# Kernel optimization log

Measured on AMD Instinct MI355X. Metric: run time of the kernel, lower is better.

## Reference

```python
import jax, jax.numpy as jnp
import numpy as np

B, T, D = 1024, 512, 64   # batch, seq_len, input_dim
H, L, OUT = 8, 3, 1       # hidden (mid_dim), num_layers, output_dim


def setup_inputs() -> dict:
    key = jax.random.key(0)
    ks = jax.random.split(key, 18)
    s = 1.0 / np.sqrt(H)  # torch LSTM default init scale
    u = lambda k, shape: jax.random.uniform(k, shape, jnp.float32, -s, s)
    return {
        "input_seq": jax.random.normal(ks[0], (B, T, D), jnp.float32),
        "h0": jax.random.normal(ks[1], (L, B, H), jnp.float32),
        "c0": jax.random.normal(ks[2], (L, B, H), jnp.float32),
        # encoder LSTM params (layer0 input dim differs)
        "enc_Wih0": u(ks[3], (4 * H, D)),
        "enc_Wih_rest": u(ks[4], (L - 1, 4 * H, H)),
        "enc_Whh": u(ks[5], (L, 4 * H, H)),
        "enc_bih": u(ks[6], (L, 4 * H)),
        "enc_bhh": u(ks[7], (L, 4 * H)),
        # decoder LSTM params
        "dec_Wih0": u(ks[8], (4 * H, D)),
        "dec_Wih_rest": u(ks[9], (L - 1, 4 * H, H)),
        "dec_Whh": u(ks[10], (L, 4 * H, H)),
        "dec_bih": u(ks[11], (L, 4 * H)),
        "dec_bhh": u(ks[12], (L, 4 * H)),
        # decoder output projection
        "lin_W": u(ks[13], (OUT, H)),
        "lin_b": u(ks[14], (OUT,)),
    }


def _cell(x, h, c, Wih, Whh, b):
    # one LSTM cell step, torch gate order: i, f, g, o
    gates = x @ Wih.T + h @ Whh.T + b  # [B, 4H]
    i, f, g, o = jnp.split(gates, 4, axis=-1)
    c2 = jax.nn.sigmoid(f) * c + jax.nn.sigmoid(i) * jnp.tanh(g)
    h2 = jax.nn.sigmoid(o) * jnp.tanh(c2)
    return h2, c2


def _stack_step(h, c, x_t, Wih0, Wih_rest, Whh, bih, bhh):
    # one timestep through all L layers; h, c: [L, B, H]
    hs, cs = [], []
    inp = x_t
    for l in range(L):
        Wih = Wih0 if l == 0 else Wih_rest[l - 1]
        h_l, c_l = _cell(inp, h[l], c[l], Wih, Whh[l], bih[l] + bhh[l])
        hs.append(h_l)
        cs.append(c_l)
        inp = h_l
    return jnp.stack(hs), jnp.stack(cs)


def reference(input_seq, h0, c0, enc_Wih0, enc_Wih_rest, enc_Whh, enc_bih, enc_bhh,
              dec_Wih0, dec_Wih_rest, dec_Whh, dec_bih, dec_bhh, lin_W, lin_b):
    x_tbd = jnp.transpose(input_seq, (1, 0, 2))  # [T, B, D] for scan

    # Encoder: full-sequence 3-layer LSTM, keep final (h, c)
    def enc_step(carry, x_t):
        h, c = carry
        h2, c2 = _stack_step(h, c, x_t, enc_Wih0, enc_Wih_rest, enc_Whh, enc_bih, enc_bhh)
        return (h2, c2), None

    (h, c), _ = jax.lax.scan(enc_step, (h0, c0), x_tbd)

    # Decoder: one LSTM step per timestep, fed the input at that step
    def dec_step(carry, x_t):
        h, c = carry
        h2, c2 = _stack_step(h, c, x_t, dec_Wih0, dec_Wih_rest, dec_Whh, dec_bih, dec_bhh)
        return (h2, c2), None

    (h, c), _ = jax.lax.scan(dec_step, (h, c), x_tbd)

    # original returns outputs[:, -1, :] = linear applied to last decoder output
    pred_last = h[-1] @ lin_W.T + lin_b  # [B, OUT]
    return pred_last
```

## Files before the change

kernel.cpp:

```cpp
#include <hip/hip_runtime.h>

#define TT 512
#define DD 64
#define BB 1024
#define PF 8
#define HH 8

typedef float v2f __attribute__((ext_vector_type(2)));

__device__ __forceinline__ float fexp2(float x){ return __builtin_amdgcn_exp2f(x); }
__device__ __forceinline__ float frcp (float x){ return __builtin_amdgcn_rcpf(x); }

template<int C>
__device__ __forceinline__ float dppf(float x){
  return __int_as_float(__builtin_amdgcn_update_dpp(0, __float_as_int(x), C, 0xF, 0xF, true));
}
template<int C>
__device__ __forceinline__ int dppi(int x){
  return __builtin_amdgcn_update_dpp(0, x, C, 0xF, 0xF, true);
}

__device__ __forceinline__ float swz16(float x){
  return __int_as_float(__builtin_amdgcn_ds_swizzle(__float_as_int(x), 0x401F));
}

template<int N> struct IC { static constexpr int v = N; };

__global__ __launch_bounds__(256) void proj_kernel(
    const float* __restrict__ x,
    const float* __restrict__ eWih0, const float* __restrict__ eBih, const float* __restrict__ eBhh,
    const float* __restrict__ dWih0, const float* __restrict__ dBih, const float* __restrict__ dBhh,
    float* __restrict__ P)
{
  __shared__ __align__(16) float xs[4][2][16 * 64];
  const int tid  = threadIdx.x;
  const int w    = tid >> 6;
  const int lane = tid & 63;
  const int ph   = lane >> 5;
  const int r    = lane & 31;
  const float* W = ph ? dWih0 : eWih0;
  const float b0 = ph ? (dBih[r] + dBhh[r]) : (eBih[r] + eBhh[r]);
  const int gate = r >> 3, j = r & 7;
  const int pos  = (gate * 4 + (j & 3)) * 2 + (j >> 2);

  float Wx[64];
#pragma unroll
  for (int k = 0; k < 16; ++k) {
    float4 wq = *(const float4*)(W + r * 64 + k * 4);
    Wx[k*4+0] = wq.x; Wx[k*4+1] = wq.y; Wx[k*4+2] = wq.z; Wx[k*4+3] = wq.w;
  }

  const int base_row = (blockIdx.x * 4 + w) * 64;
  const float* xg = x + (size_t)base_row * 64;

  float4 st[4];
#pragma unroll
  for (int i = 0; i < 4; ++i) st[i] = *(const float4*)(xg + i * 256 + lane * 4);
#pragma unroll
  for (int i = 0; i < 4; ++i) *(float4*)&xs[w][0][i * 256 + lane * 4] = st[i];
#pragma unroll
  for (int i = 0; i < 4; ++i) st[i] = *(const float4*)(xg + 1024 + i * 256 + lane * 4);

#pragma unroll 1
  for (int g = 0; g < 4; ++g) {
    const float* buf = &xs[w][g & 1][0];
#pragma unroll 2
    for (int ri = 0; ri < 16; ++ri) {
      float a0 = b0, a1 = 0.f, a2 = 0.f, a3 = 0.f;
#pragma unroll
      for (int kc = 0; kc < 16; ++kc) {
        float4 xv = *(const float4*)(buf + ri * 64 + kc * 4);
        a0 = fmaf(Wx[kc*4+0], xv.x, a0);
        a1 = fmaf(Wx[kc*4+1], xv.y, a1);
        a2 = fmaf(Wx[kc*4+2], xv.z, a2);
        a3 = fmaf(Wx[kc*4+3], xv.w, a3);
      }
      const int row = base_row + g * 16 + ri;
      const int e = row >> 9, t = row & 511;
      P[((size_t)((ph << 10) + e) * TT + t) * 32 + pos] = (a0 + a1) + (a2 + a3);
    }
    if (g < 3) {
#pragma unroll
      for (int i = 0; i < 4; ++i) *(float4*)&xs[w][(g + 1) & 1][i * 256 + lane * 4] = st[i];
      if (g < 2) {
#pragma unroll
        for (int i = 0; i < 4; ++i)
          st[i] = *(const float4*)(xg + (size_t)(g + 2) * 1024 + i * 256 + lane * 4);
      }
    }
  }
}

__global__ __launch_bounds__(128) void recur_kernel(
    const float* __restrict__ P,
    const float* __restrict__ h0,    const float* __restrict__ c0,
    const float* __restrict__ eWihR, const float* __restrict__ eWhh,
    const float* __restrict__ eBih,  const float* __restrict__ eBhh,
    const float* __restrict__ dWihR, const float* __restrict__ dWhh,
    const float* __restrict__ dBih,  const float* __restrict__ dBhh,
    const float* __restrict__ linW,  const float* __restrict__ linB,
    float* __restrict__ out)
{
  const int tid = threadIdx.x;
  const int idx = tid & 31;
  const int v   = idx >> 2;
  const int g   = idx & 3;
  const int b   = v & 3;
  const bool rB = (v >= 4);
  const int e   = blockIdx.x * 4 + (tid >> 5);

  const bool is_tanh = (g == 2);
  const float ns_act = is_tanh ? -2.885390082f : -1.44269504f;
  const float a_act  = is_tanh ? 2.0f : 1.0f;
  const float b_act  = is_tanh ? -1.0f : 0.0f;

  const int qidx = (tid >> 2) & 3;
  const int p4 = dppi<0x124>(qidx);
  const int d  = __builtin_amdgcn_readfirstlane((p4 - qidx) & 3);

  float H[3], cs[3], sd[3];
  float bd1 = 0.f, bd2 = 0.f;
  float WS[3][8], WB[2][8], Bss[2];

#pragma unroll
  for (int l = 0; l < 3; ++l) {
    H[l]  = h0[((size_t)l * BB + e) * HH + v];
    cs[l] = c0[((size_t)l * BB + e) * HH + v];
  }

  auto bcast = [&](float hn, float* A, float* Bv) {
    float Hsw = swz16(hn);
    float Lo = rB ? Hsw : hn;
    float Hi = rB ? hn : Hsw;
    A[0]  = Lo; A[1]  = dppf<0x124>(Lo); A[2]  = dppf<0x128>(Lo); A[3]  = dppf<0x12C>(Lo);
    Bv[0] = Hi; Bv[1] = dppf<0x124>(Hi); Bv[2] = dppf<0x128>(Hi); Bv[3] = dppf<0x12C>(Hi);
  };

  auto load_phase = [&](const float* WihR, const float* Whh,
                        const float* Bih, const float* Bhh) {
#pragma unroll
    for (int l = 0; l < 3; ++l) {
      const int r0 = l * 32 + g * 8 + v;
#pragma unroll
      for (int k = 0; k < 4; ++k) {
        const int col = (b + d * k) & 3;
        WS[l][k]     = Whh[r0 * 8 + col];
        WS[l][4 + k] = Whh[r0 * 8 + 4 + col];
      }
    }
#pragma unroll
    for (int l = 0; l < 2; ++l) {
      const int r0 = l * 32 + g * 8 + v;
#pragma unroll
      for (int k = 0; k < 4; ++k) {
        const int col = (b + d * k) & 3;
        WB[l][k]     = WihR[r0 * 8 + col];
        WB[l][4 + k] = WihR[r0 * 8 + 4 + col];
      }
      Bss[l] = Bih[(l + 1) * 32 + g * 8 + v] + Bhh[(l + 1) * 32 + g * 8 + v];
    }
#pragma unroll
    for (int l = 0; l < 3; ++l) {
      float A[4], Bv[4];
      bcast(H[l], A, Bv);
      float acc = l ? Bss[l - 1] : 0.f;
#pragma unroll
      for (int k = 0; k < 4; ++k) {
        acc = fmaf(WS[l][k],     A[k],  acc);
        acc = fmaf(WS[l][4 + k], Bv[k], acc);
      }
      sd[l] = acc;
    }
  };

  auto lstep = [&](auto LC, float in) -> float {
    constexpr int l = decltype(LC)::v;
    float pre = in + sd[l];
    float ex  = fexp2(ns_act * pre);
    float rc  = frcp(1.f + ex);
    float act = fmaf(a_act, rc, b_act);
    float Gi = dppf<0x00>(act);
    float Gf = dppf<0x55>(act);
    float Gg = dppf<0xAA>(act);
    float Go = dppf<0xFF>(act);
    float cn = fmaf(Gf, cs[l], Gi * Gg);
    cs[l] = cn;
    float tx = fexp2(-2.885390082f * cn);
    float tr = frcp(1.f + tx);
    float th = fmaf(2.f, tr, -1.f);
    float hn = Go * th;
    H[l] = hn;
    float A[4], Bv[4];
    bcast(hn, A, Bv);
    float accS;
    if constexpr (l > 0) accS = Bss[l - 1]; else accS = 0.f;
#pragma unroll
    for (int k = 0; k < 4; ++k) {
      accS = fmaf(WS[l][k],     A[k],  accS);
      accS = fmaf(WS[l][4 + k], Bv[k], accS);
    }
    sd[l] = accS;
    float accB = 0.f;
    if constexpr (l < 2) {
#pragma unroll
      for (int k = 0; k < 4; ++k) {
        accB = fmaf(WB[l][k],     A[k],  accB);
        accB = fmaf(WB[l][4 + k], Bv[k], accB);
      }
    }
    return accB;
  };

#pragma unroll 1
  for (int ph = 0; ph < 2; ++ph) {
    if (ph == 0) load_phase(eWihR, eWhh, eBih, eBhh);
    else         load_phase(dWihR, dWhh, dBih, dBhh);

    const int pos = (g * 4 + b) * 2 + (v >> 2);
    const float* Pb = P + ((size_t)((ph << 10) + e) * TT) * 32 + pos;

    float pf[PF];
#pragma unroll
    for (int k = 0; k < PF; ++k) pf[k] = Pb[k * 32];

#pragma unroll
    for (int k = 0; k < PF; ++k) {
      float cur = pf[k];
      pf[k] = Pb[(k + PF) * 32];
      float n1 = lstep(IC<0>{}, cur);
      float n2 = 0.f;
      if (k >= 1) n2 = lstep(IC<1>{}, bd1);
      if (k >= 2) (void)lstep(IC<2>{}, bd2);
      bd1 = n1; bd2 = n2;
    }

#pragma unroll 1
    for (int t = PF; t < TT; t += PF) {
#pragma unroll
      for (int k = 0; k < PF; ++k) {
        float cur = pf[k];
        int tn = t + k + PF; if (tn > TT - 1) tn = TT - 1;
        pf[k] = Pb[(size_t)tn * 32];
        float n1 = lstep(IC<0>{}, cur);
        float n2 = lstep(IC<1>{}, bd1);
        (void)lstep(IC<2>{}, bd2);
        bd1 = n1; bd2 = n2;
      }
    }

    float dd = lstep(IC<1>{}, bd1);
    (void)lstep(IC<2>{}, bd2);
    (void)lstep(IC<2>{}, dd);
  }

  float lwA[4], lwB[4];
#pragma unroll
  for (int k = 0; k < 4; ++k) {
    const int col = (b + d * k) & 3;
    lwA[k] = linW[col];
    lwB[k] = linW[4 + col];
  }
  float A[4], Bv[4];
  bcast(H[2], A, Bv);
  float pred = linB[0];
#pragma unroll
  for (int k = 0; k < 4; ++k) {
    pred = fmaf(lwA[k], A[k],  pred);
    pred = fmaf(lwB[k], Bv[k], pred);
  }
  if (idx == 0) out[e] = pred;
}

__global__ __launch_bounds__(64) void seq2seq_fallback(
    const float* __restrict__ x, const float* __restrict__ h0, const float* __restrict__ c0,
    const float* __restrict__ eWih0, const float* __restrict__ eWihR, const float* __restrict__ eWhh,
    const float* __restrict__ eBih,  const float* __restrict__ eBhh,
    const float* __restrict__ dWih0, const float* __restrict__ dWihR, const float* __restrict__ dWhh,
    const float* __restrict__ dBih,  const float* __restrict__ dBhh,
    const float* __restrict__ linW,  const float* __restrict__ linB, float* __restrict__ out)
{
  const int tid = threadIdx.x;
  const int g   = tid & 31;
  const int grp = tid & 32;
  const int jj  = g & 7;
  const int e   = blockIdx.x * 2 + (tid >> 5);
  const bool is_tanh = ((g >> 3) == 2);
  const float s_act = is_tanh ? 2.885390082f : 1.44269504f;
  const float a_act = is_tanh ? 2.0f : 1.0f;
  const float b_act = is_tanh ? -1.0f : 0.0f;
  float hrep[3][8]; float cc[3];
#pragma unroll
  for (int l = 0; l < 3; ++l) {
#pragma unroll
    for (int k = 0; k < 8; ++k) hrep[l][k] = h0[((size_t)l * BB + e) * HH + k];
    cc[l] = c0[((size_t)l * BB + e) * HH + jj];
  }
  for (int p = 0; p < 2; ++p) {
    const float* Wih0 = p ? dWih0 : eWih0;  const float* WihR = p ? dWihR : eWihR;
    const float* Whh  = p ? dWhh  : eWhh;   const float* Bih  = p ? dBih  : eBih;
    const float* Bhh  = p ? dBhh  : eBhh;
    float Wx[64];
#pragma unroll
    for (int k = 0; k < 64; k += 4) {
      float4 w = *(const float4*)(Wih0 + g * 64 + k);
      Wx[k] = w.x; Wx[k+1] = w.y; Wx[k+2] = w.z; Wx[k+3] = w.w;
    }
    float Wh[3][8], Wi[2][8], bias[3];
#pragma unroll
    for (int l = 0; l < 3; ++l) {
#pragma unroll
      for (int k = 0; k < 8; ++k) Wh[l][k] = Whh[(l*32+g)*8+k];
      bias[l] = Bih[l*32+g] + Bhh[l*32+g];
    }
#pragma unroll
    for (int l = 0; l < 2; ++l)
#pragma unroll
      for (int k = 0; k < 8; ++k) Wi[l][k] = WihR[(l*32+g)*8+k];
    const float* xrow = x + (size_t)e * TT * DD;
    for (int t = 0; t < TT; ++t) {
      float4 acc = make_float4(bias[0], 0.f, 0.f, 0.f);
#pragma unroll
      for (int kc = 0; kc < 16; ++kc) {
        float4 xv = *(const float4*)(xrow + kc * 4);
        acc.x = fmaf(Wx[kc*4+0], xv.x, acc.x); acc.y = fmaf(Wx[kc*4+1], xv.y, acc.y);
        acc.z = fmaf(Wx[kc*4+2], xv.z, acc.z); acc.w = fmaf(Wx[kc*4+3], xv.w, acc.w);
      }
      float pre = (acc.x + acc.y) + (acc.z + acc.w);
      { float r0=0.f,r1=0.f;
#pragma unroll
        for (int k = 0; k < 8; k += 2) { r0=fmaf(Wh[0][k],hrep[0][k],r0); r1=fmaf(Wh[0][k+1],hrep[0][k+1],r1); }
        pre += r0 + r1; }
#pragma unroll
      for (int l = 0; l < 3; ++l) {
        if (l > 0) {
          float r0 = bias[l], r1 = 0.f;
#pragma unroll
          for (int k = 0; k < 8; k += 2) {
            r0=fmaf(Wi[l-1][k],hrep[l-1][k],r0); r1=fmaf(Wi[l-1][k+1],hrep[l-1][k+1],r1);
            r0=fmaf(Wh[l][k],hrep[l][k],r0);     r1=fmaf(Wh[l][k+1],hrep[l][k+1],r1);
          }
          pre = r0 + r1;
        }
        float act = fmaf(a_act, frcp(1.0f + fexp2(-s_act * pre)), b_act);
        float iv = __shfl(act, grp + jj);
        float fv = __shfl(act, grp + 8 + jj);
        float gv = __shfl(act, grp + 16 + jj);
        float ov = __shfl(act, grp + 24 + jj);
        float cn = fmaf(fv, cc[l], iv * gv);
        cc[l] = cn;
        float th = fmaf(2.0f, frcp(1.0f + fexp2(-2.885390082f * cn)), -1.0f);
        float hn = ov * th;
#pragma unroll
        for (int k = 0; k < 8; ++k) hrep[l][k] = __shfl(hn, grp + k);
      }
      xrow += DD;
    }
  }
  float pred = linB[0];
#pragma unroll
  for (int k = 0; k < 8; ++k) pred = fmaf(linW[k], hrep[2][k], pred);
  if (g == 0) out[e] = pred;
}

extern "C" void kernel_launch(void* const* d_in, const int* in_sizes, int n_in,
                              void* d_out, int out_size, void* d_ws, size_t ws_size,
                              hipStream_t stream) {
  const float* x     = (const float*)d_in[0];
  const float* h0    = (const float*)d_in[1];
  const float* c0    = (const float*)d_in[2];
  const float* eWih0 = (const float*)d_in[3];
  const float* eWihR = (const float*)d_in[4];
  const float* eWhh  = (const float*)d_in[5];
  const float* eBih  = (const float*)d_in[6];
  const float* eBhh  = (const float*)d_in[7];
  const float* dWih0 = (const float*)d_in[8];
  const float* dWihR = (const float*)d_in[9];
  const float* dWhh  = (const float*)d_in[10];
  const float* dBih  = (const float*)d_in[11];
  const float* dBhh  = (const float*)d_in[12];
  const float* linW  = (const float*)d_in[13];
  const float* linB  = (const float*)d_in[14];
  float* out = (float*)d_out;

  const size_t P_BYTES = (size_t)2 * BB * TT * 32 * sizeof(float);
  if (ws_size >= P_BYTES) {
    float* P = (float*)d_ws;
    proj_kernel<<<2048, 256, 0, stream>>>(x, eWih0, eBih, eBhh, dWih0, dBih, dBhh, P);
    recur_kernel<<<BB / 4, 128, 0, stream>>>(P, h0, c0, eWihR, eWhh, eBih, eBhh,
                                             dWihR, dWhh, dBih, dBhh, linW, linB, out);
  } else {
    seq2seq_fallback<<<BB / 2, 64, 0, stream>>>(x, h0, c0, eWih0, eWihR, eWhh, eBih, eBhh,
                                                dWih0, dWihR, dWhh, dBih, dBhh, linW, linB, out);
  }
}
```

Before: 607.1 us.

## Rewrite projection as per-row dot products and interleave three LSTM layer steps

The projection kernel now has each lane hold one input row in registers and read weights directly from global memory (broadcast across the wave), writing float4 results. This drops the LDS staging and double buffering. The recurrence main loop uses a hand-interleaved lstep3 that computes all three wavefront-skewed layers together, exposing ILP across the exp, rcp and DPP latency chains. The last prefetch block is peeled so the clamp on the prefetch index is no longer needed. Register pressure rises in both kernels, and the weight loads in projection may become uniform global loads.

Measured after the change: 667.9 us. +10.0%, slower.

```diff
diff --git a/kernel.cpp b/kernel.cpp
--- a/kernel.cpp
+++ b/kernel.cpp
@@ -5,8 +5,6 @@
 #define BB 1024
 #define PF 8
 #define HH 8
-
-typedef float v2f __attribute__((ext_vector_type(2)));
 
 __device__ __forceinline__ float fexp2(float x){ return __builtin_amdgcn_exp2f(x); }
 __device__ __forceinline__ float frcp (float x){ return __builtin_amdgcn_rcpf(x); }
@@ -32,61 +30,48 @@
     const float* __restrict__ dWih0, const float* __restrict__ dBih, const float* __restrict__ dBhh,
     float* __restrict__ P)
 {
-  __shared__ __align__(16) float xs[4][2][16 * 64];
   const int tid  = threadIdx.x;
   const int w    = tid >> 6;
   const int lane = tid & 63;
-  const int ph   = lane >> 5;
-  const int r    = lane & 31;
-  const float* W = ph ? dWih0 : eWih0;
-  const float b0 = ph ? (dBih[r] + dBhh[r]) : (eBih[r] + eBhh[r]);
-  const int gate = r >> 3, j = r & 7;
-  const int pos  = (gate * 4 + (j & 3)) * 2 + (j >> 2);
-
-  float Wx[64];
-#pragma unroll
-  for (int k = 0; k < 16; ++k) {
-    float4 wq = *(const float4*)(W + r * 64 + k * 4);
-    Wx[k*4+0] = wq.x; Wx[k*4+1] = wq.y; Wx[k*4+2] = wq.z; Wx[k*4+3] = wq.w;
-  }
-
-  const int base_row = (blockIdx.x * 4 + w) * 64;
-  const float* xg = x + (size_t)base_row * 64;
-
-  float4 st[4];
-#pragma unroll
-  for (int i = 0; i < 4; ++i) st[i] = *(const float4*)(xg + i * 256 + lane * 4);
-#pragma unroll
-  for (int i = 0; i < 4; ++i) *(float4*)&xs[w][0][i * 256 + lane * 4] = st[i];
-#pragma unroll
-  for (int i = 0; i < 4; ++i) st[i] = *(const float4*)(xg + 1024 + i * 256 + lane * 4);
+  const int row  = (blockIdx.x * 4 + w) * 64 + lane;
+  const int e = row >> 9, t = row & 511;
+
+  float xr[64];
+  const float* xrow = x + (size_t)row * 64;
+#pragma unroll
+  for (int kq = 0; kq < 16; ++kq) {
+    float4 xv = *(const float4*)(xrow + kq * 4);
+    xr[kq*4+0] = xv.x; xr[kq*4+1] = xv.y; xr[kq*4+2] = xv.z; xr[kq*4+3] = xv.w;
+  }
+
+#pragma unroll
+  for (int ph = 0; ph < 2; ++ph) {
+    const float* W  = ph ? dWih0 : eWih0;
+    const float* Bi = ph ? dBih  : eBih;
+    const float* Bh = ph ? dBhh  : eBhh;
+    float* Prow = P + ((size_t)((ph << 10) + e) * TT + t) * 32;
 
 #pragma unroll 1
-  for (int g = 0; g < 4; ++g) {
-    const float* buf = &xs[w][g & 1][0];
-#pragma unroll 2
-    for (int ri = 0; ri < 16; ++ri) {
-      float a0 = b0, a1 = 0.f, a2 = 0.f, a3 = 0.f;
-#pragma unroll
-      for (int kc = 0; kc < 16; ++kc) {
-        float4 xv = *(const float4*)(buf + ri * 64 + kc * 4);
-        a0 = fmaf(Wx[kc*4+0], xv.x, a0);
-        a1 = fmaf(Wx[kc*4+1], xv.y, a1);
-        a2 = fmaf(Wx[kc*4+2], xv.z, a2);
-        a3 = fmaf(Wx[kc*4+3], xv.w, a3);
-      }
-      const int row = base_row + g * 16 + ri;
-      const int e = row >> 9, t = row & 511;
-      P[((size_t)((ph << 10) + e) * TT + t) * 32 + pos] = (a0 + a1) + (a2 + a3);
-    }
-    if (g < 3) {
-#pragma unroll
-      for (int i = 0; i < 4; ++i) *(float4*)&xs[w][(g + 1) & 1][i * 256 + lane * 4] = st[i];
-      if (g < 2) {
-#pragma unroll
-        for (int i = 0; i < 4; ++i)
-          st[i] = *(const float4*)(xg + (size_t)(g + 2) * 1024 + i * 256 + lane * 4);
-      }
+    for (int pq = 0; pq < 8; ++pq) {
+      float res[4];
+#pragma unroll
+      for (int sub = 0; sub < 4; ++sub) {
+        const int p = pq * 4 + sub;
+        const int r = (p >> 3) * 8 + (p & 1) * 4 + ((p >> 1) & 3);
+        const float* Wr = W + r * 64;
+        float a0 = Bi[r] + Bh[r], a1 = 0.f, a2 = 0.f, a3 = 0.f;
+#pragma unroll
+        for (int kq = 0; kq < 16; ++kq) {
+          float4 wv = *(const float4*)(Wr + kq * 4);
+          a0 = fmaf(wv.x, xr[kq*4+0], a0);
+          a1 = fmaf(wv.y, xr[kq*4+1], a1);
+          a2 = fmaf(wv.z, xr[kq*4+2], a2);
+          a3 = fmaf(wv.w, xr[kq*4+3], a3);
+        }
+        res[sub] = (a0 + a1) + (a2 + a3);
+      }
+      float4 st; st.x = res[0]; st.y = res[1]; st.z = res[2]; st.w = res[3];
+      *(float4*)(Prow + pq * 4) = st;
     }
   }
 }
@@ -211,6 +196,72 @@
     return accB;
   };
 
+  auto lstep3 = [&](float in0, float in1, float in2, float& nb1, float& nb2) {
+    float pre0 = in0 + sd[0];
+    float pre1 = in1 + sd[1];
+    float pre2 = in2 + sd[2];
+    float ex0 = fexp2(ns_act * pre0);
+    float ex1 = fexp2(ns_act * pre1);
+    float ex2 = fexp2(ns_act * pre2);
+    float rc0 = frcp(1.f + ex0);
+    float rc1 = frcp(1.f + ex1);
+    float rc2 = frcp(1.f + ex2);
+    float ac0 = fmaf(a_act, rc0, b_act);
+    float ac1 = fmaf(a_act, rc1, b_act);
+    float ac2 = fmaf(a_act, rc2, b_act);
+    float Gi0 = dppf<0x00>(ac0), Gi1 = dppf<0x00>(ac1), Gi2 = dppf<0x00>(ac2);
+    float Gf0 = dppf<0x55>(ac0), Gf1 = dppf<0x55>(ac1), Gf2 = dppf<0x55>(ac2);
+    float Gg0 = dppf<0xAA>(ac0), Gg1 = dppf<0xAA>(ac1), Gg2 = dppf<0xAA>(ac2);
+    float Go0 = dppf<0xFF>(ac0), Go1 = dppf<0xFF>(ac1), Go2 = dppf<0xFF>(ac2);
+    float cn0 = fmaf(Gf0, cs[0], Gi0 * Gg0);
+    float cn1 = fmaf(Gf1, cs[1], Gi1 * Gg1);
+    float cn2 = fmaf(Gf2, cs[2], Gi2 * Gg2);
+    cs[0] = cn0; cs[1] = cn1; cs[2] = cn2;
+    float tx0 = fexp2(-2.885390082f * cn0);
+    float tx1 = fexp2(-2.885390082f * cn1);
+    float tx2 = fexp2(-2.885390082f * cn2);
+    float tr0 = frcp(1.f + tx0);
+    float tr1 = frcp(1.f + tx1);
+    float tr2 = frcp(1.f + tx2);
+    float th0 = fmaf(2.f, tr0, -1.f);
+    float th1 = fmaf(2.f, tr1, -1.f);
+    float th2 = fmaf(2.f, tr2, -1.f);
+    float hn0 = Go0 * th0;
+    float hn1 = Go1 * th1;
+    float hn2 = Go2 * th2;
+    H[0] = hn0; H[1] = hn1; H[2] = hn2;
+    float sw0 = swz16(hn0);
+    float sw1 = swz16(hn1);
+    float sw2 = swz16(hn2);
+    float Lo0 = rB ? sw0 : hn0, Hi0 = rB ? hn0 : sw0;
+    float Lo1 = rB ? sw1 : hn1, Hi1 = rB ? hn1 : sw1;
+    float Lo2 = rB ? sw2 : hn2, Hi2 = rB ? hn2 : sw2;
+    float A0[4], B0[4], A1[4], B1[4], A2[4], B2[4];
+    A0[0] = Lo0; A0[1] = dppf<0x124>(Lo0); A0[2] = dppf<0x128>(Lo0); A0[3] = dppf<0x12C>(Lo0);
+    B0[0] = Hi0; B0[1] = dppf<0x124>(Hi0); B0[2] = dppf<0x128>(Hi0); B0[3] = dppf<0x12C>(Hi0);
+    A1[0] = Lo1; A1[1] = dppf<0x124>(Lo1); A1[2] = dppf<0x128>(Lo1); A1[3] = dppf<0x12C>(Lo1);
+    B1[0] = Hi1; B1[1] = dppf<0x124>(Hi1); B1[2] = dppf<0x128>(Hi1); B1[3] = dppf<0x12C>(Hi1);
+    A2[0] = Lo2; A2[1] = dppf<0x124>(Lo2); A2[2] = dppf<0x128>(Lo2); A2[3] = dppf<0x12C>(Lo2);
+    B2[0] = Hi2; B2[1] = dppf<0x124>(Hi2); B2[2] = dppf<0x128>(Hi2); B2[3] = dppf<0x12C>(Hi2);
+    float s0 = 0.f, s1 = Bss[0], s2 = Bss[1];
+    float u0 = 0.f, u1 = 0.f;
+#pragma unroll
+    for (int k = 0; k < 4; ++k) {
+      s0 = fmaf(WS[0][k],     A0[k], s0);
+      s0 = fmaf(WS[0][4 + k], B0[k], s0);
+      s1 = fmaf(WS[1][k],     A1[k], s1);
+      s1 = fmaf(WS[1][4 + k], B1[k], s1);
+      s2 = fmaf(WS[2][k],     A2[k], s2);
+      s2 = fmaf(WS[2][4 + k], B2[k], s2);
+      u0 = fmaf(WB[0][k],     A0[k], u0);
+      u0 = fmaf(WB[0][4 + k], B0[k], u0);
+      u1 = fmaf(WB[1][k],     A1[k], u1);
+      u1 = fmaf(WB[1][4 + k], B1[k], u1);
+    }
+    sd[0] = s0; sd[1] = s1; sd[2] = s2;
+    nb1 = u0; nb2 = u1;
+  };
+
 #pragma unroll 1
   for (int ph = 0; ph < 2; ++ph) {
     if (ph == 0) load_phase(eWihR, eWhh, eBih, eBhh);
@@ -235,17 +286,23 @@
     }
 
 #pragma unroll 1
-    for (int t = PF; t < TT; t += PF) {
+    for (int t = PF; t < TT - PF; t += PF) {
+      const float* Pq = Pb + (size_t)(t + PF) * 32;
 #pragma unroll
       for (int k = 0; k < PF; ++k) {
         float cur = pf[k];
-        int tn = t + k + PF; if (tn > TT - 1) tn = TT - 1;
-        pf[k] = Pb[(size_t)tn * 32];
-        float n1 = lstep(IC<0>{}, cur);
-        float n2 = lstep(IC<1>{}, bd1);
-        (void)lstep(IC<2>{}, bd2);
+        pf[k] = Pq[k * 32];
+        float n1, n2;
+        lstep3(cur, bd1, bd2, n1, n2);
         bd1 = n1; bd2 = n2;
       }
+    }
+#pragma unroll
+    for (int k = 0; k < PF; ++k) {
+      float cur = pf[k];
+      float n1, n2;
+      lstep3(cur, bd1, bd2, n1, n2);
+      bd1 = n1; bd2 = n2;
     }
 
     float dd = lstep(IC<1>{}, bd1);
```
